# Kernel tuning notes

Hardware: AMD Instinct MI355X
Metric: run time of the kernel (lower is better)

## Reference

```python
import jax, jax.numpy as jnp
import numpy as np

B = 16384; T = 12; MLP = 1024; ZD = 32; H = 128; NSG = 4
N_STATE = 6; NPRED = 2; DT = 0.4 * 4


def _linear_init(k, out_d, in_d):
    s = 1.0 / np.sqrt(in_d)
    kw, kb = jax.random.split(k)
    W = jax.random.uniform(kw, (out_d, in_d), minval=-s, maxval=s, dtype=jnp.float32)
    b = jax.random.uniform(kb, (out_d,), minval=-s, maxval=s, dtype=jnp.float32)
    return W, b


def setup_inputs() -> dict:
    key = jax.random.key(0)
    ks = jax.random.split(key, 16)
    W_dec_hidden, b_dec_hidden = _linear_init(ks[0], H, MLP + ZD)
    W_to_vel, b_to_vel = _linear_init(ks[1], NPRED, N_STATE)
    W_ih, b_ih = _linear_init(ks[2], 3 * H, MLP + ZD + 2 * NPRED)
    W_hh, b_hh = _linear_init(ks[3], 3 * H, H)
    W_mu, b_mu = _linear_init(ks[4], NPRED, H)
    W_std, b_std = _linear_init(ks[5], NPRED, H)
    W_sg, b_sg = _linear_init(ks[6], NPRED, 4)
    return {
        'last_obs_st': jax.random.normal(ks[7], (B, N_STATE), dtype=jnp.float32),
        'last_obs_pos': jax.random.normal(ks[8], (B, 2), dtype=jnp.float32),
        'enc_h_feat': jax.random.normal(ks[9], (B, MLP), dtype=jnp.float32),
        'z': jax.random.normal(ks[10], (B, ZD), dtype=jnp.float32),
        'sg': jax.random.normal(ks[11], (B, NSG, 2), dtype=jnp.float32),
        'fut_traj': jax.random.normal(ks[12], (T, B, N_STATE), dtype=jnp.float32),
        'sg_update_idx': jnp.array([0, 3, 7, 11], dtype=jnp.int32),
        'W_dec_hidden': W_dec_hidden, 'b_dec_hidden': b_dec_hidden,
        'W_to_vel': W_to_vel, 'b_to_vel': b_to_vel,
        'W_ih': W_ih, 'b_ih': b_ih, 'W_hh': W_hh, 'b_hh': b_hh,
        'W_mu': W_mu, 'b_mu': b_mu, 'W_std': W_std, 'b_std': b_std,
        'W_sg': W_sg, 'b_sg': b_sg,
    }


def reference(last_obs_st, last_obs_pos, enc_h_feat, z, sg, fut_traj, sg_update_idx,
              W_dec_hidden, b_dec_hidden, W_to_vel, b_to_vel, W_ih, b_ih,
              W_hh, b_hh, W_mu, b_mu, W_std, b_std, W_sg, b_sg):
    upd = np.asarray(sg_update_idx)  # static control-flow schedule
    zx = jnp.concatenate([enc_h_feat, z], axis=1)              # [B, MLP+ZD]
    h0 = zx @ W_dec_hidden.T + b_dec_hidden                    # [B, H]
    a0 = last_obs_st @ W_to_vel.T + b_to_vel                   # [B, 2]

    pts = jnp.concatenate([last_obs_pos[:, None], sg], axis=1)  # [B, 1+NSG, 2]
    pts = (pts - pts[:, :1]) / 100.0
    v = (pts[:, 1:] - pts[:, :-1]) / DT                         # [B, NSG, 2]
    sg_state = jnp.concatenate([pts[:, 1:], v], axis=-1)        # [B, NSG, 4]
    sg_feat_upd = jnp.einsum('bjf,of->jbo', sg_state, W_sg) + b_sg  # [NSG, B, 2]

    # sg_feat held constant between update steps (matches python-loop gating)
    j_idx = np.clip(np.searchsorted(upd, np.arange(T), side='right') - 1, 0, len(upd) - 1)
    sg_feat_all = sg_feat_upd[j_idx]                            # [T, B, 2]

    # teacher forcing: a for step i>0 is fut_traj[i-1,:,2:4]
    a_seq = jnp.concatenate([a0[None], fut_traj[:-1, :, 2:4]], axis=0)  # [T, B, 2]

    # precompute input-side GRU gate projections (zx part is step-invariant)
    D = zx.shape[1]
    gates_zx = zx @ W_ih[:, :D].T                               # [B, 3H]
    gates_a = jnp.einsum('tbi,gi->tbg', a_seq, W_ih[:, D:D + 2])
    gates_sg = jnp.einsum('tbi,gi->tbg', sg_feat_all, W_ih[:, D + 2:])
    gates_x = gates_zx[None] + gates_a + gates_sg + b_ih        # [T, B, 3H]

    def step(h, gx):
        gh = h @ W_hh.T + b_hh
        r = jax.nn.sigmoid(gx[:, :H] + gh[:, :H])
        zg = jax.nn.sigmoid(gx[:, H:2 * H] + gh[:, H:2 * H])
        n = jnp.tanh(gx[:, 2 * H:] + r * gh[:, 2 * H:])
        h_new = (1.0 - zg) * n + zg * h
        mu = h_new @ W_mu.T + b_mu
        std = jnp.sqrt(jnp.exp(h_new @ W_std.T + b_std))
        return h_new, (mu, std)

    _, (mus, stds) = jax.lax.scan(step, h0, gates_x)
    return mus, stds  # each [T, B, 2] — params of returned Normal
```

## Files before the change

kernel.cpp:

```cpp
#include <hip/hip_runtime.h>
#include <hip/hip_bf16.h>

#define BN 16384
#define TT 12
#define MLP 1024
#define ZD 32
#define HD 128
#define KD 1056
#define GN 384
#define WIH_LD 1060
#define NSG 4
#define DTC 1.6f
#define PLD 512
#define SLD 40
#define GRU_ROWS 16

typedef __attribute__((ext_vector_type(8))) short short8;
typedef __attribute__((ext_vector_type(4))) short short4_t;
typedef __attribute__((ext_vector_type(4))) float floatx4;
typedef __hip_bfloat16 bf16;

__device__ __forceinline__ float bf2f(bf16 v) { return __bfloat162float(v); }
__device__ __forceinline__ bf16 f2bf(float v) { return __float2bfloat16(v); }
__device__ __forceinline__ short bfbits(float x) {
    bf16 t = __float2bfloat16(x);
    return __builtin_bit_cast(short, t);
}
__device__ __forceinline__ float bfraw2f(unsigned short u) {
    return __uint_as_float(((unsigned int)u) << 16);
}
__device__ __forceinline__ float sigm(float x) {
    return __builtin_amdgcn_rcpf(1.0f + __expf(-x));
}
__device__ __forceinline__ float tanh_f(float x) {
    return 1.0f - 2.0f * __builtin_amdgcn_rcpf(1.0f + __expf(2.0f * x));
}
__device__ __forceinline__ short8 pack8(floatx4 a, floatx4 b) {
    short8 v;
    v[0]=bfbits(a[0]); v[1]=bfbits(a[1]); v[2]=bfbits(a[2]); v[3]=bfbits(a[3]);
    v[4]=bfbits(b[0]); v[5]=bfbits(b[1]); v[6]=bfbits(b[2]); v[7]=bfbits(b[3]);
    return v;
}
__device__ __forceinline__ short8 ld8f(const float* q) {
    return pack8(*(const floatx4*)q, *(const floatx4*)(q + 4));
}
__device__ __forceinline__ void barrier_lgkm() {
    asm volatile("s_waitcnt lgkmcnt(0)\n\ts_barrier" ::: "memory");
}

__global__ __launch_bounds__(512, 4) void k_gemm(
    const float* __restrict__ enc, const float* __restrict__ zz,
    const float* __restrict__ Wih, const float* __restrict__ Wdec,
    const float* __restrict__ bih, const float* __restrict__ bhh,
    const float* __restrict__ bdec,
    bf16* __restrict__ P)
{
    __shared__ __align__(16) bf16 sA[2][128 * SLD];
    __shared__ __align__(16) bf16 sB[2][128 * SLD];
    const int tid = threadIdx.x;
    const int lane = tid & 63;
    const int wav = tid >> 6;
    const int wm2 = wav >> 2;
    const int wn2 = wav & 3;
    const int c = lane & 15;
    const int quad = lane >> 4;
    const int m0 = blockIdx.x * 128;
    const int n0 = blockIdx.y * 128;

    const int srow = tid >> 2;
    const int scq = (tid & 3) * 8;
    const int nn = n0 + srow;
    const float* arow = enc + (size_t)(m0 + srow) * MLP + scq;
    const float* zrow = zz + (size_t)(m0 + srow) * ZD + scq;
    const float* brow = (nn < GN) ? Wih + (size_t)nn * WIH_LD + scq
                                  : Wdec + (size_t)(nn - GN) * KD + scq;

    floatx4 pa[2][2], pb[2][2];
#pragma unroll
    for (int s0 = 0; s0 < 2; s0++) {
        const float* qa = arow + s0 * 32;
        const float* qb = brow + s0 * 32;
        pa[s0][0] = *(const floatx4*)qa; pa[s0][1] = *(const floatx4*)(qa + 4);
        pb[s0][0] = *(const floatx4*)qb; pb[s0][1] = *(const floatx4*)(qb + 4);
    }

    float bias[2];
#pragma unroll
    for (int j = 0; j < 2; j++) {
        const int n = n0 + wn2 * 32 + j * 16 + c;
        bias[j] = (n < GN) ? (bih[n] + (n < 256 ? bhh[n] : 0.0f)) : bdec[n - GN];
    }

    floatx4 acc[4][2];
#pragma unroll
    for (int i = 0; i < 4; i++)
#pragma unroll
        for (int j = 0; j < 2; j++) acc[i][j] = floatx4{0.f, 0.f, 0.f, 0.f};

    for (int kc = 0; kc < 33; kc++) {
        const int sl = kc & 1;
        *(short8*)&sA[sl][srow * SLD + scq] = pack8(pa[sl][0], pa[sl][1]);
        *(short8*)&sB[sl][srow * SLD + scq] = pack8(pb[sl][0], pb[sl][1]);
        if (kc + 2 < 33) {
            const int k2 = (kc + 2) * 32;
            const float* qa = (kc + 2 < 32) ? arow + k2 : zrow;
            const float* qb = brow + k2;
            pa[sl][0] = *(const floatx4*)qa; pa[sl][1] = *(const floatx4*)(qa + 4);
            pb[sl][0] = *(const floatx4*)qb; pb[sl][1] = *(const floatx4*)(qb + 4);
        }
        barrier_lgkm();
        short8 a[4], b[2];
#pragma unroll
        for (int i = 0; i < 4; i++)
            a[i] = *(const short8*)&sA[sl][(wm2 * 64 + i * 16 + c) * SLD + quad * 8];
#pragma unroll
        for (int j = 0; j < 2; j++)
            b[j] = *(const short8*)&sB[sl][(wn2 * 32 + j * 16 + c) * SLD + quad * 8];
#pragma unroll
        for (int i = 0; i < 4; i++)
#pragma unroll
            for (int j = 0; j < 2; j++)
                acc[i][j] = __builtin_amdgcn_mfma_f32_16x16x32_bf16(
                    a[i], b[j], acc[i][j], 0, 0, 0);
    }
#pragma unroll
    for (int i = 0; i < 4; i++)
#pragma unroll
        for (int j = 0; j < 2; j++)
#pragma unroll
            for (int r = 0; r < 4; r++)
                P[(size_t)(m0 + wm2 * 64 + i * 16 + quad * 4 + r) * PLD
                  + n0 + wn2 * 32 + j * 16 + c] = f2bf(acc[i][j][r] + bias[j]);
}

struct SMem {
    bf16 pst[GRU_ROWS][520];
    bf16 h[2][GRU_ROWS][136];
    bf16 ext[TT][GRU_ROWS][4];
    float sgf[NSG][GRU_ROWS][2];
    float a0[GRU_ROWS][2];
    float muw[4][132];
    float b4[4];
};

__device__ __forceinline__ void heads_out(const SMem& s, float* __restrict__ out,
                                          int rows0, int t, int buf, int tid) {
    const int row = tid >> 2;
    const int sel = tid & 3;
    float sum = 0.0f;
#pragma unroll
    for (int k8 = 0; k8 < 16; k8++) {
        short8 hv = *(const short8*)(&s.h[buf][row][k8 * 8]);
#pragma unroll
        for (int u = 0; u < 8; u++)
            sum += bfraw2f((unsigned short)hv[u]) * s.muw[sel][k8 * 8 + u];
    }
    sum += s.b4[sel];
    const size_t TB2 = (size_t)TT * BN * 2;
    const size_t grow = (size_t)rows0 + row;
    if (sel < 2) out[((size_t)t * BN + grow) * 2 + sel] = sum;
    else out[TB2 + ((size_t)t * BN + grow) * 2 + (sel - 2)] = __expf(0.5f * sum);
}

__global__ __launch_bounds__(256, 2) void k_gru(
    const float* __restrict__ lst, const float* __restrict__ lpos,
    const float* __restrict__ sg, const float* __restrict__ fut,
    const int* __restrict__ updp,
    const float* __restrict__ Wtv, const float* __restrict__ btv,
    const float* __restrict__ Wih,
    const float* __restrict__ Whh, const float* __restrict__ bhh,
    const float* __restrict__ Wmu, const float* __restrict__ bmu,
    const float* __restrict__ Wstd, const float* __restrict__ bstd,
    const float* __restrict__ Wsg, const float* __restrict__ bsg,
    const bf16* __restrict__ P, float* __restrict__ out)
{
    __shared__ __align__(16) SMem s;
    const int tid = threadIdx.x;
    const int lane = tid & 63;
    const int wav = tid >> 6;
    const int c = lane & 15;
    const int quad = lane >> 4;
    const int d = blockIdx.x;
    const int b = 8 * (d & 7) + 64 * (d >> 6) + ((d >> 3) & 7);
    const int rows0 = b * GRU_ROWS;
    const int jb = wav * 32;

#pragma unroll
    for (int it = 0; it < 4; it++) {
        const int idx = it * 256 + tid;
        const int row = idx >> 6;
        const int col8 = idx & 63;
        *(short8*)&s.pst[row][col8 * 8] =
            *(const short8*)&P[(size_t)(rows0 + row) * PLD + col8 * 8];
    }

#pragma unroll
    for (int u = tid; u < 512; u += 256) {
        int sel = u >> 7, k = u & 127;
        s.muw[sel][k] = (sel < 2) ? Wmu[sel * 128 + k] : Wstd[(sel - 2) * 128 + k];
    }
    if (tid < 4) s.b4[tid] = (tid < 2) ? bmu[tid] : bstd[tid - 2];
    if (tid < GRU_ROWS) {
        const int row = rows0 + tid;
        for (int pp = 0; pp < 2; pp++) {
            float sum = btv[pp];
            for (int f = 0; f < 6; f++)
                sum += lst[(size_t)row * 6 + f] * Wtv[pp * 6 + f];
            s.a0[tid][pp] = sum;
        }
        float px = lpos[(size_t)row * 2];
        float py = lpos[(size_t)row * 2 + 1];
        float prevx = 0.f, prevy = 0.f;
        for (int j = 0; j < NSG; j++) {
            float rx = (sg[((size_t)row * NSG + j) * 2] - px) * 0.01f;
            float ry = (sg[((size_t)row * NSG + j) * 2 + 1] - py) * 0.01f;
            float vx = (rx - prevx) * (1.0f / DTC), vy = (ry - prevy) * (1.0f / DTC);
            prevx = rx; prevy = ry;
            float st4[4] = {rx, ry, vx, vy};
            for (int pp = 0; pp < 2; pp++) {
                float sum = bsg[pp];
                for (int f = 0; f < 4; f++) sum += st4[f] * Wsg[pp * 4 + f];
                s.sgf[j][tid][pp] = sum;
            }
        }
    }
    int upd[4];
#pragma unroll
    for (int i = 0; i < 4; i++) upd[i] = updp[i];

    short8 Wb[2][3][4];
    short8 Wb4[2][2];
    float Wa2[2][2], Ws2[2][2], bhh2[2];
#pragma unroll
    for (int jt2 = 0; jt2 < 2; jt2++) {
#pragma unroll
        for (int g = 0; g < 3; g++) {
            const int n = g * 128 + jb + jt2 * 16 + c;
#pragma unroll
            for (int kc = 0; kc < 4; kc++)
                Wb[jt2][g][kc] = ld8f(Whh + (size_t)n * HD + kc * 32 + quad * 8);
            if (g < 2) {
                short8 v = {0, 0, 0, 0, 0, 0, 0, 0};
                if (quad == 0) {
                    const float* q = Wih + (size_t)n * WIH_LD + KD;
                    v[0] = bfbits(q[0]); v[1] = bfbits(q[1]);
                    v[2] = bfbits(q[2]); v[3] = bfbits(q[3]);
                }
                Wb4[jt2][g] = v;
            }
        }
        const int n2 = 256 + jb + jt2 * 16 + c;
        const float* q2 = Wih + (size_t)n2 * WIH_LD + KD;
        Wa2[jt2][0] = q2[0]; Wa2[jt2][1] = q2[1];
        Ws2[jt2][0] = q2[2]; Ws2[jt2][1] = q2[3];
        bhh2[jt2] = bhh[n2];
    }

    __syncthreads();

    floatx4 gzx[2][3];
#pragma unroll
    for (int jt2 = 0; jt2 < 2; jt2++) {
#pragma unroll
        for (int g = 0; g < 3; g++) {
            const int n = g * 128 + jb + jt2 * 16 + c;
            floatx4 v;
#pragma unroll
            for (int r = 0; r < 4; r++) {
                const int mrow = quad * 4 + r;
                v[r] = bf2f(s.pst[mrow][n]);
            }
            gzx[jt2][g] = v;
        }
    }
    float hreg[2][4];
#pragma unroll
    for (int jt2 = 0; jt2 < 2; jt2++) {
        const int hcol = jb + jt2 * 16 + c;
#pragma unroll
        for (int r = 0; r < 4; r++) {
            const int mrow = quad * 4 + r;
            float hv = bf2f(s.pst[mrow][GN + hcol]);
            hreg[jt2][r] = hv;
            s.h[1][mrow][hcol] = f2bf(hv);
        }
    }
    if (tid < TT * GRU_ROWS) {
        const int t = tid >> 4, row = tid & (GRU_ROWS - 1);
        float a0v, a1v;
        if (t == 0) { a0v = s.a0[row][0]; a1v = s.a0[row][1]; }
        else {
            const float* fp = fut + ((size_t)(t - 1) * BN + rows0 + row) * 6 + 2;
            a0v = fp[0]; a1v = fp[1];
        }
        int jj = 0;
#pragma unroll
        for (int q = 1; q < NSG; q++) if (upd[q] <= t) jj = q;
        s.ext[t][row][0] = f2bf(a0v);
        s.ext[t][row][1] = f2bf(a1v);
        s.ext[t][row][2] = f2bf(s.sgf[jj][row][0]);
        s.ext[t][row][3] = f2bf(s.sgf[jj][row][1]);
    }
    __syncthreads();

    for (int t = 0; t < TT; t++) {
        const int bi = (t & 1) ^ 1;
        const int bo = t & 1;

        floatx4 acc[2][3];
#pragma unroll
        for (int jt2 = 0; jt2 < 2; jt2++) {
            acc[jt2][0] = gzx[jt2][0];
            acc[jt2][1] = gzx[jt2][1];
            floatx4 bb; bb[0] = bb[1] = bb[2] = bb[3] = bhh2[jt2];
            acc[jt2][2] = bb;
        }
#pragma unroll
        for (int kc = 0; kc < 4; kc++) {
            short8 am = *(const short8*)(&s.h[bi][c][kc * 32 + quad * 8]);
#pragma unroll
            for (int jt2 = 0; jt2 < 2; jt2++)
#pragma unroll
                for (int g = 0; g < 3; g++)
                    acc[jt2][g] = __builtin_amdgcn_mfma_f32_16x16x32_bf16(
                        am, Wb[jt2][g][kc], acc[jt2][g], 0, 0, 0);
        }
        {
            short8 am4 = {0, 0, 0, 0, 0, 0, 0, 0};
            if (quad == 0) {
                short4_t e = *(const short4_t*)(&s.ext[t][c][0]);
                am4[0] = e[0]; am4[1] = e[1]; am4[2] = e[2]; am4[3] = e[3];
            }
#pragma unroll
            for (int jt2 = 0; jt2 < 2; jt2++)
#pragma unroll
                for (int g = 0; g < 2; g++)
                    acc[jt2][g] = __builtin_amdgcn_mfma_f32_16x16x32_bf16(
                        am4, Wb4[jt2][g], acc[jt2][g], 0, 0, 0);
        }

        if (t > 0 && tid < 64) heads_out(s, out, rows0, t - 1, bi, tid);

#pragma unroll
        for (int r = 0; r < 4; r++) {
            const int mrow = quad * 4 + r;
            short4_t e4 = *(const short4_t*)(&s.ext[t][mrow][0]);
            float a0v = bfraw2f((unsigned short)e4[0]);
            float a1v = bfraw2f((unsigned short)e4[1]);
            float s0v = bfraw2f((unsigned short)e4[2]);
            float s1v = bfraw2f((unsigned short)e4[3]);
#pragma unroll
            for (int jt2 = 0; jt2 < 2; jt2++) {
                float rr = sigm(acc[jt2][0][r]);
                float zg = sigm(acc[jt2][1][r]);
                float tn = a0v * Wa2[jt2][0] + a1v * Wa2[jt2][1]
                         + s0v * Ws2[jt2][0] + s1v * Ws2[jt2][1];
                float narg = gzx[jt2][2][r] + tn + rr * acc[jt2][2][r];
                float nn = tanh_f(narg);
                float hv = nn + zg * (hreg[jt2][r] - nn);
                hreg[jt2][r] = hv;
                s.h[bo][mrow][jb + jt2 * 16 + c] = f2bf(hv);
            }
        }
        barrier_lgkm();
    }
    if (tid < 64) heads_out(s, out, rows0, TT - 1, (TT - 1) & 1, tid);
}

extern "C" void kernel_launch(void* const* d_in, const int* in_sizes, int n_in,
                              void* d_out, int out_size, void* d_ws, size_t ws_size,
                              hipStream_t stream) {
    const float* lst  = (const float*)d_in[0];
    const float* lpos = (const float*)d_in[1];
    const float* enc  = (const float*)d_in[2];
    const float* zz   = (const float*)d_in[3];
    const float* sg   = (const float*)d_in[4];
    const float* fut  = (const float*)d_in[5];
    const int*   upd  = (const int*)d_in[6];
    const float* Wdec = (const float*)d_in[7];
    const float* bdec = (const float*)d_in[8];
    const float* Wtv  = (const float*)d_in[9];
    const float* btv  = (const float*)d_in[10];
    const float* Wih  = (const float*)d_in[11];
    const float* bih  = (const float*)d_in[12];
    const float* Whh  = (const float*)d_in[13];
    const float* bhh  = (const float*)d_in[14];
    const float* Wmu  = (const float*)d_in[15];
    const float* bmu  = (const float*)d_in[16];
    const float* Wstd = (const float*)d_in[17];
    const float* bstd = (const float*)d_in[18];
    const float* Wsg  = (const float*)d_in[19];
    const float* bsg  = (const float*)d_in[20];
    float* out = (float*)d_out;

    bf16* P = (bf16*)d_ws;
    k_gemm<<<dim3(128, 4), 512, 0, stream>>>(enc, zz, Wih, Wdec, bih, bhh, bdec, P);
    k_gru<<<BN / GRU_ROWS, 256, 0, stream>>>(
        lst, lpos, sg, fut, upd, Wtv, btv, Wih, Whh, bhh,
        Wmu, bmu, Wstd, bstd, Wsg, bsg, P, out);
}
```

Before: 255.1 us.

## Compute GRU output heads with MFMA and remap GEMM blocks across XCDs

```diff
diff --git a/kernel.cpp b/kernel.cpp
--- a/kernel.cpp
+++ b/kernel.cpp
@@ -64,8 +64,11 @@
     const int wn2 = wav & 3;
     const int c = lane & 15;
     const int quad = lane >> 4;
-    const int m0 = blockIdx.x * 128;
-    const int n0 = blockIdx.y * 128;
+    const int d = blockIdx.x;
+    const int xcd = d & 7;
+    const int slot = d >> 3;
+    const int m0 = ((slot >> 2) * 8 + xcd) * 128;
+    const int n0 = (slot & 3) * 128;
 
     const int srow = tid >> 2;
     const int scq = (tid & 3) * 8;
@@ -139,28 +142,7 @@
     bf16 ext[TT][GRU_ROWS][4];
     float sgf[NSG][GRU_ROWS][2];
     float a0[GRU_ROWS][2];
-    float muw[4][132];
-    float b4[4];
 };
-
-__device__ __forceinline__ void heads_out(const SMem& s, float* __restrict__ out,
-                                          int rows0, int t, int buf, int tid) {
-    const int row = tid >> 2;
-    const int sel = tid & 3;
-    float sum = 0.0f;
-#pragma unroll
-    for (int k8 = 0; k8 < 16; k8++) {
-        short8 hv = *(const short8*)(&s.h[buf][row][k8 * 8]);
-#pragma unroll
-        for (int u = 0; u < 8; u++)
-            sum += bfraw2f((unsigned short)hv[u]) * s.muw[sel][k8 * 8 + u];
-    }
-    sum += s.b4[sel];
-    const size_t TB2 = (size_t)TT * BN * 2;
-    const size_t grow = (size_t)rows0 + row;
-    if (sel < 2) out[((size_t)t * BN + grow) * 2 + sel] = sum;
-    else out[TB2 + ((size_t)t * BN + grow) * 2 + (sel - 2)] = __expf(0.5f * sum);
-}
 
 __global__ __launch_bounds__(256, 2) void k_gru(
     const float* __restrict__ lst, const float* __restrict__ lpos,
@@ -184,6 +166,7 @@
     const int b = 8 * (d & 7) + 64 * (d >> 6) + ((d >> 3) & 7);
     const int rows0 = b * GRU_ROWS;
     const int jb = wav * 32;
+    const size_t TB2 = (size_t)TT * BN * 2;
 
 #pragma unroll
     for (int it = 0; it < 4; it++) {
@@ -194,12 +177,6 @@
             *(const short8*)&P[(size_t)(rows0 + row) * PLD + col8 * 8];
     }
 
-#pragma unroll
-    for (int u = tid; u < 512; u += 256) {
-        int sel = u >> 7, k = u & 127;
-        s.muw[sel][k] = (sel < 2) ? Wmu[sel * 128 + k] : Wstd[(sel - 2) * 128 + k];
-    }
-    if (tid < 4) s.b4[tid] = (tid < 2) ? bmu[tid] : bstd[tid - 2];
     if (tid < GRU_ROWS) {
         const int row = rows0 + tid;
         for (int pp = 0; pp < 2; pp++) {
@@ -256,6 +233,21 @@
         bhh2[jt2] = bhh[n2];
     }
 
+    short8 mwb[4];
+    float hbias = 0.0f;
+#pragma unroll
+    for (int kc = 0; kc < 4; kc++) {
+        short8 v = {0, 0, 0, 0, 0, 0, 0, 0};
+        if (c < 4) {
+            const float* q = (c < 2 ? Wmu + (size_t)c * HD
+                                    : Wstd + (size_t)(c - 2) * HD)
+                             + kc * 32 + quad * 8;
+            v = ld8f(q);
+        }
+        mwb[kc] = v;
+    }
+    if (c < 4) hbias = (c < 2) ? bmu[c] : bstd[c - 2];
+
     __syncthreads();
 
     floatx4 gzx[2][3];
@@ -315,6 +307,7 @@
             floatx4 bb; bb[0] = bb[1] = bb[2] = bb[3] = bhh2[jt2];
             acc[jt2][2] = bb;
         }
+        floatx4 acch = floatx4{0.f, 0.f, 0.f, 0.f};
 #pragma unroll
         for (int kc = 0; kc < 4; kc++) {
             short8 am = *(const short8*)(&s.h[bi][c][kc * 32 + quad * 8]);
@@ -324,6 +317,9 @@
                 for (int g = 0; g < 3; g++)
                     acc[jt2][g] = __builtin_amdgcn_mfma_f32_16x16x32_bf16(
                         am, Wb[jt2][g][kc], acc[jt2][g], 0, 0, 0);
+            if (wav == 3)
+                acch = __builtin_amdgcn_mfma_f32_16x16x32_bf16(
+                    am, mwb[kc], acch, 0, 0, 0);
         }
         {
             short8 am4 = {0, 0, 0, 0, 0, 0, 0, 0};
@@ -339,7 +335,16 @@
                         am4, Wb4[jt2][g], acc[jt2][g], 0, 0, 0);
         }
 
-        if (t > 0 && tid < 64) heads_out(s, out, rows0, t - 1, bi, tid);
+        if (wav == 3 && c < 4 && t > 0) {
+#pragma unroll
+            for (int r = 0; r < 4; r++) {
+                const int row = quad * 4 + r;
+                const float v = acch[r] + hbias;
+                const size_t g = ((size_t)(t - 1) * BN + rows0 + row) * 2;
+                if (c < 2) out[g + c] = v;
+                else out[TB2 + g + (c - 2)] = __expf(0.5f * v);
+            }
+        }
 
 #pragma unroll
         for (int r = 0; r < 4; r++) {
@@ -364,7 +369,27 @@
         }
         barrier_lgkm();
     }
-    if (tid < 64) heads_out(s, out, rows0, TT - 1, (TT - 1) & 1, tid);
+
+    if (wav == 3) {
+        const int bf = (TT - 1) & 1;
+        floatx4 acch = floatx4{0.f, 0.f, 0.f, 0.f};
+#pragma unroll
+        for (int kc = 0; kc < 4; kc++) {
+            short8 am = *(const short8*)(&s.h[bf][c][kc * 32 + quad * 8]);
+            acch = __builtin_amdgcn_mfma_f32_16x16x32_bf16(
+                am, mwb[kc], acch, 0, 0, 0);
+        }
+        if (c < 4) {
+#pragma unroll
+            for (int r = 0; r < 4; r++) {
+                const int row = quad * 4 + r;
+                const float v = acch[r] + hbias;
+                const size_t g = ((size_t)(TT - 1) * BN + rows0 + row) * 2;
+                if (c < 2) out[g + c] = v;
+                else out[TB2 + g + (c - 2)] = __expf(0.5f * v);
+            }
+        }
+    }
 }
 
 extern "C" void kernel_launch(void* const* d_in, const int* in_sizes, int n_in,
@@ -394,7 +419,7 @@
     float* out = (float*)d_out;
 
     bf16* P = (bf16*)d_ws;
-    k_gemm<<<dim3(128, 4), 512, 0, stream>>>(enc, zz, Wih, Wdec, bih, bhh, bdec, P);
+    k_gemm<<<512, 512, 0, stream>>>(enc, zz, Wih, Wdec, bih, bhh, bdec, P);
     k_gru<<<BN / GRU_ROWS, 256, 0, stream>>>(
         lst, lpos, sg, fut, upd, Wtv, btv, Wih, Whh, bhh,
         Wmu, bmu, Wstd, bstd, Wsg, bsg, P, out);
```

Measured after the change: 254.7 us. About the same (-0.1%).
